# Performance work log

Measured on AMD Instinct MI355X. Metric: run time of the kernel, lower is better.

The kernel has to match this reference:

```python
import jax, jax.numpy as jnp
import numpy as np

B, S, E, H, SHARE = 32, 1024, 256, 256, 2


def setup_inputs() -> dict:
    key = jax.random.key(0)
    ks = jax.random.split(key, 14)
    sc_e = 1.0 / np.sqrt(E)
    sc_h = 1.0 / np.sqrt(H)
    mk = lambda k, shape, sc: (jax.random.normal(k, shape, jnp.float32) * sc)
    return {
        "inputs": jax.random.normal(ks[0], (B, S, E), jnp.float32),
        "mask": jnp.ones((B, S), jnp.float32),
        # forward-direction cell params
        "Wx": mk(ks[1], (E, 4 * H), sc_e),
        "Wh": mk(ks[2], (H, 4 * H), sc_h),
        "Ws": mk(ks[3], (H, 4 * H), sc_h),
        "b": jnp.zeros((4 * H,), jnp.float32),
        "Wrx": mk(ks[4], (SHARE, E, H), sc_e),
        "Wrh": mk(ks[5], (SHARE, H, H), sc_h),
        "br": jnp.zeros((SHARE, H), jnp.float32),
        # reverse-direction cell params (deepcopy in torch; distinct draws here)
        "Wx_r": mk(ks[6], (E, 4 * H), sc_e),
        "Wh_r": mk(ks[7], (H, 4 * H), sc_h),
        "Ws_r": mk(ks[8], (H, 4 * H), sc_h),
        "b_r": jnp.zeros((4 * H,), jnp.float32),
        "Wrx_r": mk(ks[9], (SHARE, E, H), sc_e),
        "Wrh_r": mk(ks[10], (SHARE, H, H), sc_h),
        "br_r": jnp.zeros((SHARE, H), jnp.float32),
        "idx": 1,
    }


def _run_dir(xs, ms, params, idx, reverse):
    # xs: [S,B,E] time-major, ms: [S,B]
    Wx, Wh, Ws, b, Wrx, Wrh, br = params
    if reverse:
        xs = xs[::-1]
        ms = ms[::-1]
    Bt = xs.shape[1]
    Hd = Wh.shape[0]
    K = Wrx.shape[0]
    h0 = jnp.zeros((Bt, Hd), xs.dtype)
    c0 = jnp.zeros((Bt, Hd), xs.dtype)
    s0 = jnp.zeros((K, Bt, Hd), xs.dtype)  # shared cells (init_s)

    def step(carry, xm):
        h, c, s = carry
        x_t, m_t = xm
        # gates read x, h, and the idx-selected shared cell
        z = x_t @ Wx + h @ Wh + s[idx] @ Ws + b  # [B, 4H]
        i, f, g, o = jnp.split(z, 4, axis=-1)
        c_new = jax.nn.sigmoid(f) * c + jax.nn.sigmoid(i) * jnp.tanh(g)
        h_new = jax.nn.sigmoid(o) * jnp.tanh(c_new)
        m = m_t[:, None]
        h = m * h_new + (1.0 - m) * h
        c = m * c_new + (1.0 - m) * c
        # shared-cell gates, all K at once: [K,B,H]
        r = jax.nn.sigmoid(
            jnp.einsum("be,keh->kbh", x_t, Wrx)
            + jnp.einsum("bh,khj->kbj", h, Wrh)
            + br[:, None, :]
        )
        s_new = r * s + (1.0 - r) * c[None]
        s = m[None] * s_new + (1.0 - m[None]) * s
        return (h, c, s), (h, c, s)

    _, (hs, cs, ss) = jax.lax.scan(step, (h0, c0, s0), (xs, ms))
    if reverse:
        hs, cs, ss = hs[::-1], cs[::-1], ss[::-1]
    return hs, cs, ss  # [S,B,H], [S,B,H], [S,K,B,H]


def reference(inputs, mask, Wx, Wh, Ws, b, Wrx, Wrh, br,
              Wx_r, Wh_r, Ws_r, b_r, Wrx_r, Wrh_r, br_r, idx):
    xs = inputs.transpose(1, 0, 2)  # [S,B,E]
    ms = mask.T  # [S,B]
    hs_f, cs_f, ss_f = _run_dir(xs, ms, (Wx, Wh, Ws, b, Wrx, Wrh, br), idx, False)
    hs_r, cs_r, ss_r = _run_dir(xs, ms, (Wx_r, Wh_r, Ws_r, b_r, Wrx_r, Wrh_r, br_r), idx, True)
    h_f = jnp.concatenate([hs_f, hs_r], axis=-1)  # [S,B,2H]
    c_f = jnp.concatenate([cs_f, cs_r], axis=-1)  # [S,B,2H]
    # final_list: per shared-cell index, stacked over time -> [K,S,B,2H]
    s_f = jnp.concatenate([ss_f, ss_r], axis=-1).transpose(1, 0, 2, 3)
    return (h_f, c_f, s_f)
```

## Files before the change

kernel.cpp:

```cpp
#include <hip/hip_runtime.h>
#include <hip/hip_bf16.h>
#include <cstdint>
#include <cstddef>


typedef __bf16 bf16x8 __attribute__((ext_vector_type(8)));
typedef float  f32x4  __attribute__((ext_vector_type(4)));
typedef unsigned long long u64x2 __attribute__((ext_vector_type(2)));
typedef unsigned long long u64;

#define DEVINL __device__ __forceinline__

constexpr int Ss = 1024;

constexpr size_t OFF_FLAGS = 0;
constexpr size_t OFF_H   = 4096;
constexpr size_t SZ_H    = (size_t)2*2*32*256*2;
constexpr size_t OFF_C   = OFF_H + SZ_H;
constexpr size_t SZ_C    = (size_t)2*2*32*256*4;
constexpr size_t OFF_R   = OFF_C + SZ_C;
constexpr size_t SZ_R    = (size_t)2*2*32*256*2;
constexpr size_t OFF_WH  = OFF_R + SZ_R;
constexpr size_t SZ_W    = (size_t)2*1024*256*2;
constexpr size_t OFF_WX  = OFF_WH + SZ_W;
constexpr size_t OFF_WS  = OFF_WX + SZ_W;
constexpr size_t OFF_WRX = OFF_WS + SZ_W;
constexpr size_t SZ_WR   = (size_t)2*2*256*256*2;
constexpr size_t OFF_WRH = OFF_WRX + SZ_WR;

DEVINL unsigned short f2bf(float f) {
    unsigned u = __builtin_bit_cast(unsigned, f);
    u += 0x7FFFu + ((u >> 16) & 1u);
    return (unsigned short)(u >> 16);
}
DEVINL u64 pack4(float4 v) {
    return (u64)f2bf(v.x) | ((u64)f2bf(v.y) << 16)
         | ((u64)f2bf(v.z) << 32) | ((u64)f2bf(v.w) << 48);
}
DEVINL float sigm(float x) { return 1.f / (1.f + __expf(-x)); }

DEVINL u64 ald64(const u64* p) {
    return __hip_atomic_load(p, __ATOMIC_RELAXED, __HIP_MEMORY_SCOPE_AGENT);
}
DEVINL unsigned ald32(const unsigned* p) {
    return __hip_atomic_load(p, __ATOMIC_RELAXED, __HIP_MEMORY_SCOPE_AGENT);
}
DEVINL void ast64(u64* p, u64 v) {
    __hip_atomic_store(p, v, __ATOMIC_RELAXED, __HIP_MEMORY_SCOPE_AGENT);
}
DEVINL void ast32u(unsigned* p, unsigned v) {
    __hip_atomic_store(p, v, __ATOMIC_RELAXED, __HIP_MEMORY_SCOPE_AGENT);
}

__global__ void prepass(const float* __restrict__ Wx0, const float* __restrict__ Wh0,
                        const float* __restrict__ Ws0,
                        const float* __restrict__ Wx1, const float* __restrict__ Wh1,
                        const float* __restrict__ Ws1,
                        const float* __restrict__ Wrx0, const float* __restrict__ Wrh0,
                        const float* __restrict__ Wrx1, const float* __restrict__ Wrh1,
                        unsigned char* __restrict__ ws)
{
    unsigned short* whT  = (unsigned short*)(ws + OFF_WH);
    unsigned short* wxT  = (unsigned short*)(ws + OFF_WX);
    unsigned short* wsT  = (unsigned short*)(ws + OFF_WS);
    unsigned short* wrxT = (unsigned short*)(ws + OFF_WRX);
    unsigned short* wrhT = (unsigned short*)(ws + OFF_WRH);
    int tid = blockIdx.x * blockDim.x + threadIdx.x;
    int NT  = gridDim.x * blockDim.x;
    for (int e = tid; e < 2*1024*256; e += NT) {
        int d = e >> 18, r = e & 262143, n = r >> 8, k = r & 255;
        whT[e] = f2bf((d ? Wh1 : Wh0)[k*1024 + n]);
        wxT[e] = f2bf((d ? Wx1 : Wx0)[k*1024 + n]);
        wsT[e] = f2bf((d ? Ws1 : Ws0)[k*1024 + n]);
    }
    for (int e = tid; e < 2*2*256*256; e += NT) {
        int d = e >> 17, r = e & 131071, kk = r >> 16, r2 = r & 65535;
        int j = r2 >> 8, k = r2 & 255;
        wrxT[e] = f2bf((d ? Wrx1 : Wrx0)[(kk*256 + k)*256 + j]);
        wrhT[e] = f2bf((d ? Wrh1 : Wrh0)[(kk*256 + k)*256 + j]);
    }
    if (blockIdx.x == 0 && threadIdx.x < 256) {
        unsigned* f = (unsigned*)ws;
#pragma unroll
        for (int i = 0; i < 4; ++i) f[threadIdx.x*4 + i] = 0u;
    }
}

#define FRAG_U64(Mt,kt,lqv,m) \
    ((u64*)(sA + (size_t)(((((Mt)*16+(kt))*4+(lqv))*16+(m))*8)))

__launch_bounds__(256, 1)
__global__ void bislstm(const float* __restrict__ inputs, const float* __restrict__ mask,
                        const float* __restrict__ b0,  const float* __restrict__ b1,
                        const float* __restrict__ br0, const float* __restrict__ br1,
                        const int* __restrict__ idxp,
                        unsigned char* __restrict__ ws, float* __restrict__ out)
{
    const int bid = blockIdx.x;
    const int d   = bid >> 5;
    const int g   = bid & 31;
    const int tid = threadIdx.x;
    const int wave = tid >> 6, lane = tid & 63;
    const int lm = lane & 15, lq = lane >> 4;

    __shared__ __align__(16) unsigned short sA[16384];
    __shared__ __align__(16) float cL[32][260];
    __shared__ __align__(16) unsigned short rL[32][264];
    __shared__ float zs[2][32][16];
    __shared__ float rsxS[2][32][16];
    __shared__ float rshS[32][16];
    __shared__ float sCex[32][8];
    __shared__ __align__(8) unsigned short sHb[256];
    __shared__ float mL[32];

    const unsigned short* whT  = (const unsigned short*)(ws + OFF_WH)  + (size_t)d*1024*256;
    const unsigned short* wxT  = (const unsigned short*)(ws + OFF_WX)  + (size_t)d*1024*256;
    const unsigned short* wsT  = (const unsigned short*)(ws + OFF_WS)  + (size_t)d*1024*256;
    const unsigned short* wrxT = (const unsigned short*)(ws + OFF_WRX) + (size_t)d*2*256*256;
    const unsigned short* wrhT = (const unsigned short*)(ws + OFF_WRH) + (size_t)d*2*256*256;
    u64* HbufU = (u64*)(ws + OFF_H);
    u64* CbufU = (u64*)(ws + OFF_C);
    u64* RbufU = (u64*)(ws + OFF_R);
    unsigned* flags = (unsigned*)ws + d*512;
    const int idxv = idxp[0];
    const float* bd  = d ? b1  : b0;
    const float* brd = d ? br1 : br0;

    const int zMt = wave & 1, zNt = wave >> 1;
    const int znl = zNt*16 + lm;
    const int zcol = (znl >> 3)*256 + g*8 + (znl & 7);
    const int rks = lm >> 3;
    const int rj  = g*8 + (lm & 7);

    bf16x8 whf[8], wsf[8], wxf[8], rwf[8], wbig[4][8];
#pragma unroll
    for (int kt = 0; kt < 8; ++kt) {
        whf[kt] = *(const bf16x8*)(whT + (size_t)zcol*256 + kt*32 + lq*8);
        wsf[kt] = *(const bf16x8*)(wsT + (size_t)zcol*256 + kt*32 + lq*8);
        wxf[kt] = *(const bf16x8*)(wxT + (size_t)zcol*256 + kt*32 + lq*8);
    }
    {
        const unsigned short* wrT = (wave < 2) ? wrhT : wrxT;
#pragma unroll
        for (int kt = 0; kt < 8; ++kt)
            rwf[kt] = *(const bf16x8*)(wrT + (size_t)(rks*256 + rj)*256 + kt*32 + lq*8);
    }
    float brj[16];
#pragma unroll
    for (int n = 0; n < 4; ++n) {
        const int j16 = wave*64 + n*16 + lm;
#pragma unroll
        for (int kt = 0; kt < 8; ++kt)
            wbig[n][kt] = *(const bf16x8*)(wrhT + (size_t)(idxv*256 + j16)*256 + kt*32 + lq*8);
#pragma unroll
        for (int r = 0; r < 4; ++r)
            brj[n*4 + r] = brd[idxv*256 + wave*64 + n*16 + lq*4 + r];
    }

    {
        u64* z8 = (u64*)sA;
#pragma unroll
        for (int i = 0; i < 16; ++i) z8[tid + 256*i] = 0ULL;
    }

    f32x4 zacc;
    {
        const int tx0 = d ? (Ss - 1) : 0;
        const float* xp = inputs + (((size_t)(zMt*16 + lm)*Ss + tx0) << 8) + lq*8;
        bf16x8 xf[8];
#pragma unroll
        for (int kt = 0; kt < 8; ++kt) {
            float4 v0 = *(const float4*)(xp + kt*32);
            float4 v1 = *(const float4*)(xp + kt*32 + 4);
            u64x2 pk; pk.x = pack4(v0); pk.y = pack4(v1);
            xf[kt] = __builtin_bit_cast(bf16x8, pk);
        }
        f32x4 a = {0.f, 0.f, 0.f, 0.f};
#pragma unroll
        for (int kt = 0; kt < 8; ++kt)
            a = __builtin_amdgcn_mfma_f32_16x16x32_bf16(xf[kt], wxf[kt], a, 0, 0, 0);
        zacc = a;
        if (wave >= 2) {
            f32x4 ra = {0.f, 0.f, 0.f, 0.f};
#pragma unroll
            for (int kt = 0; kt < 8; ++kt)
                ra = __builtin_amdgcn_mfma_f32_16x16x32_bf16(xf[kt], rwf[kt], ra, 0, 0, 0);
#pragma unroll
            for (int r = 0; r < 4; ++r) rsxS[0][zMt*16 + lq*4 + r][lm] = ra[r];
        }
    }
    __syncthreads();
    if (wave == 3) {
        const int b_ = lane >> 1, hf_ = lane & 1;
        float4 f4;
        f4.x = rsxS[0][b_][idxv*8 + hf_*4 + 0];
        f4.y = rsxS[0][b_][idxv*8 + hf_*4 + 1];
        f4.z = rsxS[0][b_][idxv*8 + hf_*4 + 2];
        f4.w = rsxS[0][b_][idxv*8 + hf_*4 + 3];
        ast64(RbufU + (size_t)d*2048 + (size_t)b_*64 + g*2 + hf_, pack4(f4));
    }

    const int eb = tid >> 3, ej = tid & 7;
    const int gj = g*8 + ej;
    const float bias_i = bd[gj], bias_f = bd[256+gj], bias_g = bd[512+gj], bias_o = bd[768+gj];
    const float brr0 = brd[gj], brr1 = brd[256+gj];
    float hprev = 0.f, cprev = 0.f, s1prev = 0.f;
    float sreg[2][4][4] = {};

    const unsigned short* aBase = sA + (size_t)(zMt*8192 + lq*128 + lm*8);

#pragma unroll 1
    for (int t = 0; t < Ss; ++t) {
        const int tx = d ? (Ss - 1 - t) : t;
        const int pc = t & 1, pcn = pc ^ 1;
        const unsigned want = (unsigned)(t + 1);
        const bool more = (t + 1 < Ss);

        if (tid < 32) mL[tid] = mask[(size_t)tid*Ss + tx];
        {
            f32x4 acc = zacc;
#pragma unroll
            for (int kt = 0; kt < 8; ++kt)
                acc = __builtin_amdgcn_mfma_f32_16x16x32_bf16(*(const bf16x8*)(aBase + kt*512), whf[kt], acc, 0, 0, 0);
#pragma unroll
            for (int kt = 0; kt < 8; ++kt)
                acc = __builtin_amdgcn_mfma_f32_16x16x32_bf16(*(const bf16x8*)(aBase + (8+kt)*512), wsf[kt], acc, 0, 0, 0);
#pragma unroll
            for (int r = 0; r < 4; ++r)
                zs[zNt][zMt*16 + lq*4 + r][lm] = acc[r];
        }
        __syncthreads();

        float m_, cu_, hu_;
        {
            float zi = zs[0][eb][ej]   + bias_i;
            float zf = zs[0][eb][8+ej] + bias_f;
            float zg = zs[1][eb][ej]   + bias_g;
            float zo = zs[1][eb][8+ej] + bias_o;
            float cn = sigm(zf)*cprev + sigm(zi)*tanhf(zg);
            float hn = sigm(zo)*tanhf(cn);
            m_  = mL[eb];
            cu_ = m_*cn + (1.f - m_)*cprev;
            hu_ = m_*hn + (1.f - m_)*hprev;
            cprev = cu_; hprev = hu_;
            sHb[tid] = f2bf(hu_);
            sCex[eb][ej] = cu_;
        }
        __syncthreads();

        if (wave == 0) {
            u64 pk = *(const u64*)&sHb[lane*4];
            ast64(HbufU + (size_t)(pc*2 + d)*2048 + (size_t)(lane>>1)*64 + g*2 + (lane&1), pk);
        } else if (wave == 1) {
            const int b_ = lane >> 1, hf_ = lane & 1;
            u64 p0 = *(const u64*)&sCex[b_][hf_*4];
            u64 p1 = *(const u64*)&sCex[b_][hf_*4 + 2];
            u64* cp = CbufU + (size_t)(pc*2 + d)*4096 + (size_t)b_*128 + g*4 + hf_*2;
            ast64(cp, p0); ast64(cp + 1, p1);
        }
        asm volatile("s_waitcnt vmcnt(0)" ::: "memory");
        __syncthreads();

        if (tid == 0) ast32u(flags + g*16, want);
        out[((size_t)tx*32 + eb)*512 + d*256 + gj] = hu_;
        out[16777216 + ((size_t)tx*32 + eb)*512 + d*256 + gj] = cu_;
        if (more) {
            const int txn = d ? (Ss - 2 - t) : (t + 1);
            const float* xp = inputs + (((size_t)(zMt*16 + lm)*Ss + txn) << 8) + lq*8;
            bf16x8 xf[8];
#pragma unroll
            for (int kt = 0; kt < 8; ++kt) {
                float4 v0 = *(const float4*)(xp + kt*32);
                float4 v1 = *(const float4*)(xp + kt*32 + 4);
                u64x2 pk; pk.x = pack4(v0); pk.y = pack4(v1);
                xf[kt] = __builtin_bit_cast(bf16x8, pk);
            }
            f32x4 a = {0.f, 0.f, 0.f, 0.f};
#pragma unroll
            for (int kt = 0; kt < 8; ++kt)
                a = __builtin_amdgcn_mfma_f32_16x16x32_bf16(xf[kt], wxf[kt], a, 0, 0, 0);
            zacc = a;
            if (wave >= 2) {
                f32x4 ra = {0.f, 0.f, 0.f, 0.f};
#pragma unroll
                for (int kt = 0; kt < 8; ++kt)
                    ra = __builtin_amdgcn_mfma_f32_16x16x32_bf16(xf[kt], rwf[kt], ra, 0, 0, 0);
#pragma unroll
                for (int r = 0; r < 4; ++r) rsxS[pcn][zMt*16 + lq*4 + r][lm] = ra[r];
            }
        }
        if (wave == 0) {
            for (;;) {
                unsigned v = ald32(flags + (lane & 31)*16);
                if (__ballot(v < want) == 0ULL) break;
                __builtin_amdgcn_s_sleep(1);
            }
            asm volatile("" ::: "memory");
        }
        __syncthreads();

        {
            const u64* Hs = (const u64*)(ws + OFF_H) + (size_t)(pc*2 + d)*2048;
#pragma unroll
            for (int i = 0; i < 4; ++i) {
                int b_ = (tid & 7) + 8*i;
                int jj = tid >> 3;
                u64 v0 = ald64(Hs + (size_t)b_*64 + jj*2);
                u64 v1 = ald64(Hs + (size_t)b_*64 + jj*2 + 1);
                u64x2 pk; pk.x = v0; pk.y = v1;
                *(u64x2*)FRAG_U64(b_ >> 4, jj >> 2, jj & 3, b_ & 15) = pk;
            }
            const u64* Cb = (const u64*)(ws + OFF_C) + (size_t)(pc*2 + d)*4096;
#pragma unroll
            for (int i = 0; i < 8; ++i) {
                int q = i*1024 + tid*4;
                int b_ = q >> 8, j = q & 255;
                u64x2 pk; pk.x = ald64(Cb + (q >> 1)); pk.y = ald64(Cb + (q >> 1) + 1);
                *(u64x2*)&cL[b_][j] = pk;
            }
            const u64* Rb = (const u64*)(ws + OFF_R) + (size_t)(pc*2 + d)*2048;
#pragma unroll
            for (int i = 0; i < 4; ++i) {
                int q = i*2048 + tid*8;
                int b_ = q >> 8, j = q & 255;
                u64x2 pk; pk.x = ald64(Rb + (q >> 2)); pk.y = ald64(Rb + (q >> 2) + 1);
                *(u64x2*)&rL[b_][j] = pk;
            }
        }
        __syncthreads();

        if (wave == 3 && more) {
            const int b_ = lane >> 1, hf_ = lane & 1;
            float4 f4;
            f4.x = rsxS[pcn][b_][idxv*8 + hf_*4 + 0];
            f4.y = rsxS[pcn][b_][idxv*8 + hf_*4 + 1];
            f4.z = rsxS[pcn][b_][idxv*8 + hf_*4 + 2];
            f4.w = rsxS[pcn][b_][idxv*8 + hf_*4 + 3];
            ast64(RbufU + (size_t)(pcn*2 + d)*2048 + (size_t)b_*64 + g*2 + hf_, pack4(f4));
        }
#pragma unroll
        for (int Mt = 0; Mt < 2; ++Mt) {
            bf16x8 hfB[8];
#pragma unroll
            for (int kt = 0; kt < 8; ++kt)
                hfB[kt] = *(const bf16x8*)(sA + (size_t)(Mt*8192 + kt*512 + lq*128 + lm*8));
            if (wave < 2 && Mt == wave) {
                f32x4 ra = {0.f, 0.f, 0.f, 0.f};
#pragma unroll
                for (int kt = 0; kt < 8; ++kt)
                    ra = __builtin_amdgcn_mfma_f32_16x16x32_bf16(hfB[kt], rwf[kt], ra, 0, 0, 0);
#pragma unroll
                for (int r = 0; r < 4; ++r) rshS[wave*16 + lq*4 + r][lm] = ra[r];
            }
            const int bb = Mt*16 + lm;
            const float mv = mL[bb];
#pragma unroll
            for (int n = 0; n < 4; ++n) {
                f32x4 a = {0.f, 0.f, 0.f, 0.f};
#pragma unroll
                for (int kt = 0; kt < 8; ++kt)
                    a = __builtin_amdgcn_mfma_f32_16x16x32_bf16(wbig[n][kt], hfB[kt], a, 0, 0, 0);
                const int j0 = wave*64 + n*16 + lq*4;
                float4 cv4 = *(const float4*)&cL[bb][j0];
                u64 rv64 = *(const u64*)&rL[bb][j0];
                u64 pk = 0ULL;
                float4 o4;
#pragma unroll
                for (int r = 0; r < 4; ++r) {
                    float cv = (r == 0) ? cv4.x : (r == 1) ? cv4.y : (r == 2) ? cv4.z : cv4.w;
                    float rx = __builtin_bit_cast(float, ((unsigned)(unsigned short)(rv64 >> (r*16))) << 16);
                    float rr = sigm(a[r] + rx + brj[n*4 + r]);
                    float so = sreg[Mt][n][r];
                    float sn = rr*so + (1.f - rr)*cv;
                    float su = mv*sn + (1.f - mv)*so;
                    sreg[Mt][n][r] = su;
                    pk |= (u64)f2bf(su) << (r*16);
                    if (r == 0) o4.x = su; else if (r == 1) o4.y = su; else if (r == 2) o4.z = su; else o4.w = su;
                }
                const int ktp = 8 + (j0 >> 5);
                const int lqv = (j0 >> 3) & 3;
                const int half = (j0 >> 2) & 1;
                *(u64*)(sA + (size_t)((((Mt*16 + ktp)*4 + lqv)*16 + lm)*8 + half*4)) = pk;
                if ((j0 >> 3) == g)
                    *(float4*)(out + 33554432 + (((size_t)idxv*1024 + tx)*32 + bb)*512 + d*256 + j0) = o4;
            }
        }
        __syncthreads();

        {
            const int k1 = 1 - idxv;
            float rv = rsxS[pc][eb][k1*8 + ej] + rshS[eb][k1*8 + ej] + (k1 ? brr1 : brr0);
            float rr = sigm(rv);
            float sn = rr*s1prev + (1.f - rr)*cu_;
            float su = m_*sn + (1.f - m_)*s1prev;
            s1prev = su;
            out[33554432 + (((size_t)k1*1024 + tx)*32 + eb)*512 + d*256 + gj] = su;
        }
    }
}

extern "C" void kernel_launch(void* const* d_in, const int* in_sizes, int n_in,
                              void* d_out, int out_size, void* d_ws, size_t ws_size,
                              hipStream_t stream) {
    const float* inputs = (const float*)d_in[0];
    const float* mask_  = (const float*)d_in[1];
    const float* Wx0  = (const float*)d_in[2];
    const float* Wh0  = (const float*)d_in[3];
    const float* Ws0  = (const float*)d_in[4];
    const float* b0   = (const float*)d_in[5];
    const float* Wrx0 = (const float*)d_in[6];
    const float* Wrh0 = (const float*)d_in[7];
    const float* br0  = (const float*)d_in[8];
    const float* Wx1  = (const float*)d_in[9];
    const float* Wh1  = (const float*)d_in[10];
    const float* Ws1  = (const float*)d_in[11];
    const float* b1   = (const float*)d_in[12];
    const float* Wrx1 = (const float*)d_in[13];
    const float* Wrh1 = (const float*)d_in[14];
    const float* br1  = (const float*)d_in[15];
    const int*   idxp = (const int*)d_in[16];
    unsigned char* ws = (unsigned char*)d_ws;

    hipLaunchKernelGGL(prepass, dim3(512), dim3(256), 0, stream,
                       Wx0, Wh0, Ws0, Wx1, Wh1, Ws1, Wrx0, Wrh0, Wrx1, Wrh1, ws);
    hipLaunchKernelGGL(bislstm, dim3(64), dim3(256), 0, stream,
                       inputs, mask_, b0, b1, br0, br1, idxp,
                       ws, (float*)d_out);
}
```

Baseline: 13.46 ms.

## Replace global flag barrier with per-cache-line sequence-tagged records for h/c/r exchange

Replaces the separate H/C/R global buffers plus per-block flag array with a single record region in which each 64-byte line carries its own sequence tag alongside packed h, c (split into bf16 hi/lo pairs) and r data. Producers write each line with a dwordx4 store and then set its tag, and consumers poll the tags of all lines they need before copying them directly into LDS fragments. This removes the block-level syncthreads and single flag write on the publish side and merges several gather passes into one. In exchange the poll reads many tags, correctness now depends on store ordering within a line, and c is carried as a two-term bf16 split rather than fp32.

```diff
diff --git a/kernel.cpp b/kernel.cpp
--- a/kernel.cpp
+++ b/kernel.cpp
@@ -13,14 +13,9 @@
 
 constexpr int Ss = 1024;
 
-constexpr size_t OFF_FLAGS = 0;
-constexpr size_t OFF_H   = 4096;
-constexpr size_t SZ_H    = (size_t)2*2*32*256*2;
-constexpr size_t OFF_C   = OFF_H + SZ_H;
-constexpr size_t SZ_C    = (size_t)2*2*32*256*4;
-constexpr size_t OFF_R   = OFF_C + SZ_C;
-constexpr size_t SZ_R    = (size_t)2*2*32*256*2;
-constexpr size_t OFF_WH  = OFF_R + SZ_R;
+constexpr size_t OFF_REC = 4096;
+constexpr size_t SZ_REC  = (size_t)2*2*2048*64;
+constexpr size_t OFF_WH  = OFF_REC + SZ_REC;
 constexpr size_t SZ_W    = (size_t)2*1024*256*2;
 constexpr size_t OFF_WX  = OFF_WH + SZ_W;
 constexpr size_t OFF_WS  = OFF_WX + SZ_W;
@@ -37,6 +32,7 @@
     return (u64)f2bf(v.x) | ((u64)f2bf(v.y) << 16)
          | ((u64)f2bf(v.z) << 32) | ((u64)f2bf(v.w) << 48);
 }
+DEVINL float bfhi(unsigned short h) { return __builtin_bit_cast(float, (unsigned)h << 16); }
 DEVINL float sigm(float x) { return 1.f / (1.f + __expf(-x)); }
 
 DEVINL u64 ald64(const u64* p) {
@@ -45,11 +41,11 @@
 DEVINL unsigned ald32(const unsigned* p) {
     return __hip_atomic_load(p, __ATOMIC_RELAXED, __HIP_MEMORY_SCOPE_AGENT);
 }
-DEVINL void ast64(u64* p, u64 v) {
-    __hip_atomic_store(p, v, __ATOMIC_RELAXED, __HIP_MEMORY_SCOPE_AGENT);
-}
 DEVINL void ast32u(unsigned* p, unsigned v) {
     __hip_atomic_store(p, v, __ATOMIC_RELAXED, __HIP_MEMORY_SCOPE_AGENT);
+}
+DEVINL void gst16(void* p, u64x2 v) {
+    asm volatile("global_store_dwordx4 %0, %1, off sc1" :: "v"(p), "v"(v) : "memory");
 }
 
 __global__ void prepass(const float* __restrict__ Wx0, const float* __restrict__ Wh0,
@@ -79,15 +75,7 @@
         wrxT[e] = f2bf((d ? Wrx1 : Wrx0)[(kk*256 + k)*256 + j]);
         wrhT[e] = f2bf((d ? Wrh1 : Wrh0)[(kk*256 + k)*256 + j]);
     }
-    if (blockIdx.x == 0 && threadIdx.x < 256) {
-        unsigned* f = (unsigned*)ws;
-#pragma unroll
-        for (int i = 0; i < 4; ++i) f[threadIdx.x*4 + i] = 0u;
-    }
-}
-
-#define FRAG_U64(Mt,kt,lqv,m) \
-    ((u64*)(sA + (size_t)(((((Mt)*16+(kt))*4+(lqv))*16+(m))*8)))
+}
 
 __launch_bounds__(256, 1)
 __global__ void bislstm(const float* __restrict__ inputs, const float* __restrict__ mask,
@@ -104,13 +92,14 @@
     const int lm = lane & 15, lq = lane >> 4;
 
     __shared__ __align__(16) unsigned short sA[16384];
-    __shared__ __align__(16) float cL[32][260];
+    __shared__ __align__(16) unsigned short chiL[32][264];
+    __shared__ __align__(16) unsigned short cloL[32][264];
     __shared__ __align__(16) unsigned short rL[32][264];
+    __shared__ __align__(16) unsigned pubA[32][16];
+    __shared__ __align__(16) unsigned pubB[32][4];
     __shared__ float zs[2][32][16];
     __shared__ float rsxS[2][32][16];
     __shared__ float rshS[32][16];
-    __shared__ float sCex[32][8];
-    __shared__ __align__(8) unsigned short sHb[256];
     __shared__ float mL[32];
 
     const unsigned short* whT  = (const unsigned short*)(ws + OFF_WH)  + (size_t)d*1024*256;
@@ -118,10 +107,6 @@
     const unsigned short* wsT  = (const unsigned short*)(ws + OFF_WS)  + (size_t)d*1024*256;
     const unsigned short* wrxT = (const unsigned short*)(ws + OFF_WRX) + (size_t)d*2*256*256;
     const unsigned short* wrhT = (const unsigned short*)(ws + OFF_WRH) + (size_t)d*2*256*256;
-    u64* HbufU = (u64*)(ws + OFF_H);
-    u64* CbufU = (u64*)(ws + OFF_C);
-    u64* RbufU = (u64*)(ws + OFF_R);
-    unsigned* flags = (unsigned*)ws + d*512;
     const int idxv = idxp[0];
     const float* bd  = d ? b1  : b0;
     const float* brd = d ? br1 : br0;
@@ -186,18 +171,22 @@
             for (int kt = 0; kt < 8; ++kt)
                 ra = __builtin_amdgcn_mfma_f32_16x16x32_bf16(xf[kt], rwf[kt], ra, 0, 0, 0);
 #pragma unroll
-            for (int r = 0; r < 4; ++r) rsxS[0][zMt*16 + lq*4 + r][lm] = ra[r];
+            for (int r = 0; r < 4; ++r) {
+                const int b = zMt*16 + lq*4 + r;
+                rsxS[0][b][lm] = ra[r];
+                if (rks == idxv) ((unsigned short*)pubB[b])[lm & 7] = f2bf(ra[r]);
+            }
         }
     }
     __syncthreads();
     if (wave == 3) {
-        const int b_ = lane >> 1, hf_ = lane & 1;
-        float4 f4;
-        f4.x = rsxS[0][b_][idxv*8 + hf_*4 + 0];
-        f4.y = rsxS[0][b_][idxv*8 + hf_*4 + 1];
-        f4.z = rsxS[0][b_][idxv*8 + hf_*4 + 2];
-        f4.w = rsxS[0][b_][idxv*8 + hf_*4 + 3];
-        ast64(RbufU + (size_t)d*2048 + (size_t)b_*64 + g*2 + hf_, pack4(f4));
+        if (lane < 32) {
+            u64x2 v = *(const u64x2*)&pubB[lane][0];
+            gst16((u64*)(ws + OFF_REC) + ((size_t)d*2048 + g*64 + lane*2 + 1)*8 + 2, v);
+        }
+        asm volatile("s_waitcnt vmcnt(0)" ::: "memory");
+        if (lane < 32)
+            ast32u((unsigned*)(ws + OFF_REC) + ((size_t)d*2048 + g*64 + lane*2 + 1)*16, 1u);
     }
 
     const int eb = tid >> 3, ej = tid & 7;
@@ -243,25 +232,29 @@
             cu_ = m_*cn + (1.f - m_)*cprev;
             hu_ = m_*hn + (1.f - m_)*hprev;
             cprev = cu_; hprev = hu_;
-            sHb[tid] = f2bf(hu_);
-            sCex[eb][ej] = cu_;
+            unsigned short chi = f2bf(cu_);
+            unsigned short clo = f2bf(cu_ - bfhi(chi));
+            unsigned short* pa = (unsigned short*)pubA[eb];
+            pa[8  + ej] = f2bf(hu_);
+            pa[16 + ej] = chi;
+            pa[24 + ej] = clo;
         }
         __syncthreads();
 
         if (wave == 0) {
-            u64 pk = *(const u64*)&sHb[lane*4];
-            ast64(HbufU + (size_t)(pc*2 + d)*2048 + (size_t)(lane>>1)*64 + g*2 + (lane&1), pk);
-        } else if (wave == 1) {
-            const int b_ = lane >> 1, hf_ = lane & 1;
-            u64 p0 = *(const u64*)&sCex[b_][hf_*4];
-            u64 p1 = *(const u64*)&sCex[b_][hf_*4 + 2];
-            u64* cp = CbufU + (size_t)(pc*2 + d)*4096 + (size_t)b_*128 + g*4 + hf_*2;
-            ast64(cp, p0); ast64(cp + 1, p1);
-        }
-        asm volatile("s_waitcnt vmcnt(0)" ::: "memory");
-        __syncthreads();
-
-        if (tid == 0) ast32u(flags + g*16, want);
+#pragma unroll
+            for (int inst = 0; inst < 2; ++inst) {
+                if ((lane & 3) != 0) {
+                    const int b = inst*16 + (lane >> 2);
+                    u64x2 v = *(const u64x2*)((const unsigned char*)pubA + inst*1024 + lane*16);
+                    gst16((u64*)(ws + OFF_REC) + ((size_t)(pc*2 + d)*16384 + ((size_t)g*64 + b*2)*8) + (lane & 3)*2, v);
+                }
+            }
+            asm volatile("s_waitcnt vmcnt(0)" ::: "memory");
+            if (lane < 32)
+                ast32u((unsigned*)(ws + OFF_REC) + (size_t)(pc*2 + d)*32768 + ((size_t)g*64 + lane*2)*16, want);
+        }
+
         out[((size_t)tx*32 + eb)*512 + d*256 + gj] = hu_;
         out[16777216 + ((size_t)tx*32 + eb)*512 + d*256 + gj] = cu_;
         if (more) {
@@ -286,57 +279,56 @@
                 for (int kt = 0; kt < 8; ++kt)
                     ra = __builtin_amdgcn_mfma_f32_16x16x32_bf16(xf[kt], rwf[kt], ra, 0, 0, 0);
 #pragma unroll
-                for (int r = 0; r < 4; ++r) rsxS[pcn][zMt*16 + lq*4 + r][lm] = ra[r];
-            }
-        }
-        if (wave == 0) {
+                for (int r = 0; r < 4; ++r) {
+                    const int b = zMt*16 + lq*4 + r;
+                    rsxS[pcn][b][lm] = ra[r];
+                    if (rks == idxv) ((unsigned short*)pubB[b])[lm & 7] = f2bf(ra[r]);
+                }
+            }
+        }
+
+        {
+            const unsigned* RecT = (const unsigned*)(ws + OFF_REC) + (size_t)(pc*2 + d)*32768;
+            const int lbase = wave*512 + lane;
             for (;;) {
-                unsigned v = ald32(flags + (lane & 31)*16);
-                if (__ballot(v < want) == 0ULL) break;
+                unsigned bad = 0;
+#pragma unroll
+                for (int i = 0; i < 8; ++i)
+                    bad |= (ald32(RecT + (size_t)(lbase + i*64)*16) != want) ? 1u : 0u;
+                if (__ballot(bad != 0u) == 0ULL) break;
                 __builtin_amdgcn_s_sleep(1);
             }
             asm volatile("" ::: "memory");
+            const u64* RecU = (const u64*)(ws + OFF_REC) + (size_t)(pc*2 + d)*16384;
+            const int role = lane & 7;
+            if (role == 1 || role == 2 || role == 3 || role == 5) {
+#pragma unroll
+                for (int i = 0; i < 32; ++i) {
+                    const int c = wave*2048 + i*64 + lane;
+                    u64x2 pk;
+                    pk.x = ald64(RecU + ((size_t)c << 1));
+                    pk.y = ald64(RecU + ((size_t)c << 1) + 1);
+                    const int line = c >> 2;
+                    const int g2 = (line >> 6) & 31, b = (line >> 1) & 31;
+                    unsigned short* dst =
+                        (role == 1) ? (sA + (size_t)((((b>>4)*16 + (g2>>2))*4 + (g2&3))*16 + (b&15))*8)
+                      : (role == 2) ? &chiL[b][g2*8]
+                      : (role == 3) ? &cloL[b][g2*8]
+                      :               &rL[b][g2*8];
+                    *(u64x2*)dst = pk;
+                }
+            }
         }
         __syncthreads();
 
-        {
-            const u64* Hs = (const u64*)(ws + OFF_H) + (size_t)(pc*2 + d)*2048;
-#pragma unroll
-            for (int i = 0; i < 4; ++i) {
-                int b_ = (tid & 7) + 8*i;
-                int jj = tid >> 3;
-                u64 v0 = ald64(Hs + (size_t)b_*64 + jj*2);
-                u64 v1 = ald64(Hs + (size_t)b_*64 + jj*2 + 1);
-                u64x2 pk; pk.x = v0; pk.y = v1;
-                *(u64x2*)FRAG_U64(b_ >> 4, jj >> 2, jj & 3, b_ & 15) = pk;
-            }
-            const u64* Cb = (const u64*)(ws + OFF_C) + (size_t)(pc*2 + d)*4096;
-#pragma unroll
-            for (int i = 0; i < 8; ++i) {
-                int q = i*1024 + tid*4;
-                int b_ = q >> 8, j = q & 255;
-                u64x2 pk; pk.x = ald64(Cb + (q >> 1)); pk.y = ald64(Cb + (q >> 1) + 1);
-                *(u64x2*)&cL[b_][j] = pk;
-            }
-            const u64* Rb = (const u64*)(ws + OFF_R) + (size_t)(pc*2 + d)*2048;
-#pragma unroll
-            for (int i = 0; i < 4; ++i) {
-                int q = i*2048 + tid*8;
-                int b_ = q >> 8, j = q & 255;
-                u64x2 pk; pk.x = ald64(Rb + (q >> 2)); pk.y = ald64(Rb + (q >> 2) + 1);
-                *(u64x2*)&rL[b_][j] = pk;
-            }
-        }
-        __syncthreads();
-
         if (wave == 3 && more) {
-            const int b_ = lane >> 1, hf_ = lane & 1;
-            float4 f4;
-            f4.x = rsxS[pcn][b_][idxv*8 + hf_*4 + 0];
-            f4.y = rsxS[pcn][b_][idxv*8 + hf_*4 + 1];
-            f4.z = rsxS[pcn][b_][idxv*8 + hf_*4 + 2];
-            f4.w = rsxS[pcn][b_][idxv*8 + hf_*4 + 3];
-            ast64(RbufU + (size_t)(pcn*2 + d)*2048 + (size_t)b_*64 + g*2 + hf_, pack4(f4));
+            if (lane < 32) {
+                u64x2 v = *(const u64x2*)&pubB[lane][0];
+                gst16((u64*)(ws + OFF_REC) + ((size_t)(pcn*2 + d)*16384 + ((size_t)g*64 + lane*2 + 1)*8) + 2, v);
+            }
+            asm volatile("s_waitcnt vmcnt(0)" ::: "memory");
+            if (lane < 32)
+                ast32u((unsigned*)(ws + OFF_REC) + (size_t)(pcn*2 + d)*32768 + ((size_t)g*64 + lane*2 + 1)*16, want + 1);
         }
 #pragma unroll
         for (int Mt = 0; Mt < 2; ++Mt) {
@@ -361,14 +353,15 @@
                 for (int kt = 0; kt < 8; ++kt)
                     a = __builtin_amdgcn_mfma_f32_16x16x32_bf16(wbig[n][kt], hfB[kt], a, 0, 0, 0);
                 const int j0 = wave*64 + n*16 + lq*4;
-                float4 cv4 = *(const float4*)&cL[bb][j0];
-                u64 rv64 = *(const u64*)&rL[bb][j0];
+                const u64 hi64 = *(const u64*)&chiL[bb][j0];
+                const u64 lo64 = *(const u64*)&cloL[bb][j0];
+                const u64 rv64 = *(const u64*)&rL[bb][j0];
                 u64 pk = 0ULL;
                 float4 o4;
 #pragma unroll
                 for (int r = 0; r < 4; ++r) {
-                    float cv = (r == 0) ? cv4.x : (r == 1) ? cv4.y : (r == 2) ? cv4.z : cv4.w;
-                    float rx = __builtin_bit_cast(float, ((unsigned)(unsigned short)(rv64 >> (r*16))) << 16);
+                    float cv = bfhi((unsigned short)(hi64 >> (r*16))) + bfhi((unsigned short)(lo64 >> (r*16)));
+                    float rx = bfhi((unsigned short)(rv64 >> (r*16)));
                     float rr = sigm(a[r] + rx + brj[n*4 + r]);
                     float so = sreg[Mt][n][r];
                     float sn = rr*so + (1.f - rr)*cv;
```

Measured after the change: 17.42 ms. +29.4%, slower.
